# Performance work log

Measured on AMD Instinct MI355X. Metric: run time of the kernel, lower is better.

The kernel has to match this reference:

```python
import jax, jax.numpy as jnp
from jax import lax
import numpy as np

NPOINT1, RADIUS1, NSAMPLE1 = 2048, 0.4, 32
NPOINT2, RADIUS2, NSAMPLE2 = 512, 0.8, 64


def _fps(xyz, npoint):
    # Farthest point sampling (deterministic start at index 0). xyz: (N,3)
    N = xyz.shape[0]
    def step(carry, _):
        dists, farthest = carry
        centroid = xyz[farthest]                      # (3,)
        d = jnp.sum((xyz - centroid) ** 2, axis=-1)   # (N,)
        dists = jnp.minimum(dists, d)
        return (dists, jnp.argmax(dists).astype(jnp.int32)), farthest
    init = (jnp.full((N,), 1e10, xyz.dtype), jnp.asarray(0, jnp.int32))
    _, idx = lax.scan(step, init, None, length=npoint)
    return idx                                        # (npoint,) int32


def _ball_query(radius, nsample, xyz, new_xyz):
    # For each centroid pick up to nsample neighbor indices within radius,
    # padding with the first found index (centroid itself is always in range).
    N = xyz.shape[0]
    sqr = jnp.sum((new_xyz[:, None, :] - xyz[None, :, :]) ** 2, axis=-1)  # (S,N)
    cand = jnp.where(sqr <= radius * radius,
                     jnp.arange(N, dtype=jnp.int32)[None, :], N)
    neg, _ = lax.top_k(-cand, nsample)   # smallest nsample valid indices
    idx = -neg
    first = idx[:, :1]
    return jnp.where(idx == N, first, idx)            # (S, nsample)


def _mlp(h, ws, bs, contract):
    # Per-point shared MLP (1x1 conv + folded-BN bias + ReLU)
    for w, b in zip(ws, bs):
        h = jax.nn.relu(jnp.einsum(contract, h, w) + b)
    return h


def _sa(xyz, feats, npoint, radius, nsample, ws, bs):
    new_xyz = xyz[_fps(xyz, npoint)]                  # (S,3)
    gidx = _ball_query(radius, nsample, xyz, new_xyz) # (S,K)
    grouped_xyz = xyz[gidx] - new_xyz[:, None, :]     # (S,K,3) centered
    h = jnp.concatenate([grouped_xyz, feats[gidx]], axis=-1)  # (S,K,3+C)
    h = _mlp(h, ws, bs, 'skc,oc->sko')
    return new_xyz, jnp.max(h, axis=1)                # (S,C_out)


def _sa_all(xyz, feats, ws, bs):
    # group_all stage: single group over all remaining points
    h = jnp.concatenate([xyz, feats], axis=-1)        # (S,3+C)
    h = _mlp(h, ws, bs, 'sc,oc->so')
    return jnp.max(h, axis=0)                         # (C_out,)


def _forward(points, proposal, w1, b1, w2, b2, w3, b3):
    x, y, w = proposal[0], proposal[1], proposal[3]
    zero = jnp.zeros_like(x)
    xyz = points - jnp.stack([x, y, zero])            # centre-normalized coords
    offs = [(x + w / 2, y), (x - w / 2, y), (x, y + w / 2), (x, y - w / 2)]
    feats = jnp.concatenate(
        [points - jnp.stack([ox, oy, zero]) for ox, oy in offs], axis=-1)  # (N,12)
    xyz1, f1 = _sa(xyz, feats, NPOINT1, RADIUS1, NSAMPLE1, w1, b1)
    xyz2, f2 = _sa(xyz1, f1, NPOINT2, RADIUS2, NSAMPLE2, w2, b2)
    return _sa_all(xyz2, f2, w3, b3)                  # (1024,)


def setup_inputs() -> dict:
    key = jax.random.key(0)
    k = jax.random.split(key, 40)
    N = 32768
    inp = {}
    inp['points'] = jax.random.normal(k[0], (N, 3), jnp.float32)
    inp['proposal'] = jax.random.uniform(k[1], (6,), jnp.float32, 0.1, 1.0)
    dims = {'sa1': [(64, 15), (64, 64), (128, 64)],
            'sa2': [(128, 131), (128, 128), (256, 128)],
            'sa3': [(256, 259), (512, 256), (1024, 512)]}
    ki = 2
    for name, layer_dims in dims.items():
        for i, (o, c) in enumerate(layer_dims):
            inp[f'{name}_w{i}'] = jax.random.normal(k[ki], (o, c), jnp.float32) / np.float32(np.sqrt(c)); ki += 1
            inp[f'{name}_b{i}'] = jax.random.normal(k[ki], (o,), jnp.float32) * 0.02; ki += 1
    return inp


def reference(points, proposal,
              sa1_w0, sa1_w1, sa1_w2, sa1_b0, sa1_b1, sa1_b2,
              sa2_w0, sa2_w1, sa2_w2, sa2_b0, sa2_b1, sa2_b2,
              sa3_w0, sa3_w1, sa3_w2, sa3_b0, sa3_b1, sa3_b2):
    return _forward(points, proposal,
                    [sa1_w0, sa1_w1, sa1_w2], [sa1_b0, sa1_b1, sa1_b2],
                    [sa2_w0, sa2_w1, sa2_w2], [sa2_b0, sa2_b1, sa2_b2],
                    [sa3_w0, sa3_w1, sa3_w2], [sa3_b0, sa3_b1, sa3_b2])
```

## Files before the change

kernel.cpp:

```cpp
#include <hip/hip_runtime.h>
#include <cstdint>
#include <cstddef>

typedef unsigned long long ull;

#define N_PTS  32768
#define NP1    2048
#define NSAMP1 32
#define NP2    512
#define NSAMP2 64

__global__ __launch_bounds__(256) void k_prep(const float* __restrict__ pts,
                                              const float* __restrict__ prop,
                                              float* __restrict__ xx,
                                              float* __restrict__ xy,
                                              float* __restrict__ xz) {
  int t = blockIdx.x * 256 + threadIdx.x;
  if (t >= N_PTS) return;
  float x = prop[0], y = prop[1];
  xx[t] = __fsub_rn(pts[3 * t + 0], x);
  xy[t] = __fsub_rn(pts[3 * t + 1], y);
  xz[t] = pts[3 * t + 2];
}

#define F1T 1024
#define F1P 32

__global__
__attribute__((amdgpu_flat_work_group_size(F1T, F1T)))
void k_fps1(const float* __restrict__ xx,
            const float* __restrict__ xy,
            const float* __restrict__ xz,
            float* __restrict__ ox,
            float* __restrict__ oy,
            float* __restrict__ oz) {
  __shared__ __align__(16) float zl[F1P * F1T];
  __shared__ float wmax[F1T / 64];
  __shared__ int S[2];
  int tid = threadIdx.x;
  char* zb = (char*)zl;
  int rowb = tid * 128 + (tid & 7) * 16;
  float px[F1P], py[F1P], d[F1P];
#pragma unroll
  for (int s = 0; s < F1P; ++s) {
    int i = s * F1T + tid;
    px[s] = xx[i];
    py[s] = xy[i];
    float z = xz[i];
    *(float*)(zb + ((rowb ^ ((s >> 2) * 16)) + (s & 3) * 4)) = z;
    d[s] = 1e10f;
  }
  if (tid == 0) { S[0] = 0; S[1] = 0x7fffffff; }
  __syncthreads();
  for (int it = 0; it < NP1; ++it) {
    int f = __builtin_amdgcn_readfirstlane(S[it & 1]);
    float cx = xx[f], cy = xy[f], cz = xz[f];
    if (tid == 0) { ox[it] = cx; oy[it] = cy; oz[it] = cz; }
    float bestv = -1.0f;
#pragma unroll
    for (int c = 0; c < 8; ++c) {
      const float4 zz = *(const float4*)(zb + (rowb ^ (c * 16)));
      float zv[4] = {zz.x, zz.y, zz.z, zz.w};
#pragma unroll
      for (int j = 0; j < 4; ++j) {
        int s = c * 4 + j;
        float dx = __fsub_rn(px[s], cx);
        float dy = __fsub_rn(py[s], cy);
        float dz = __fsub_rn(zv[j], cz);
        float d2 = __fadd_rn(__fadd_rn(__fmul_rn(dx, dx), __fmul_rn(dy, dy)), __fmul_rn(dz, dz));
        float dn = fminf(d[s], d2);
        d[s] = dn;
        bestv = fmaxf(bestv, dn);
      }
    }
    float wv = bestv;
#pragma unroll
    for (int m = 1; m < 64; m <<= 1) wv = fmaxf(wv, __shfl_xor(wv, m, 64));
    if ((tid & 63) == 0) wmax[tid >> 6] = wv;
    __syncthreads();
    float gb = wmax[0];
#pragma unroll
    for (int k = 1; k < F1T / 64; ++k) gb = fmaxf(gb, wmax[k]);
    if (bestv == gb) {
      int cand = 0x7fffffff;
#pragma unroll
      for (int s = F1P - 1; s >= 0; --s) cand = (d[s] == gb) ? (s * F1T + tid) : cand;
      atomicMin(&S[(it + 1) & 1], cand);
    }
    if (tid == 0) S[it & 1] = 0x7fffffff;
    __syncthreads();
  }
}

#define F2T 512
#define F2P 4
__global__ __launch_bounds__(F2T, 1) void k_fps2(const float* __restrict__ x1x,
                                                 const float* __restrict__ x1y,
                                                 const float* __restrict__ x1z,
                                                 float* __restrict__ ox,
                                                 float* __restrict__ oy,
                                                 float* __restrict__ oz) {
  __shared__ float sx[NP1], sy[NP1], sz[NP1];
  __shared__ float wmax[F2T / 64];
  __shared__ int S[2];
  int tid = threadIdx.x;
  float px[F2P], py[F2P], pz[F2P], d[F2P];
#pragma unroll
  for (int s = 0; s < F2P; ++s) {
    int i = s * F2T + tid;
    px[s] = x1x[i]; py[s] = x1y[i]; pz[s] = x1z[i];
    sx[i] = px[s];  sy[i] = py[s];  sz[i] = pz[s];
    d[s] = 1e10f;
  }
  if (tid == 0) { S[0] = 0; S[1] = 0x7fffffff; }
  __syncthreads();
  for (int it = 0; it < NP2; ++it) {
    int f = __builtin_amdgcn_readfirstlane(S[it & 1]);
    float cx = sx[f], cy = sy[f], cz = sz[f];
    if (tid == 0) { ox[it] = cx; oy[it] = cy; oz[it] = cz; }
    float bestv = -1.0f;
#pragma unroll
    for (int s = 0; s < F2P; ++s) {
      float dx = __fsub_rn(px[s], cx);
      float dy = __fsub_rn(py[s], cy);
      float dz = __fsub_rn(pz[s], cz);
      float d2 = __fadd_rn(__fadd_rn(__fmul_rn(dx, dx), __fmul_rn(dy, dy)), __fmul_rn(dz, dz));
      float dn = fminf(d[s], d2);
      d[s] = dn;
      bestv = fmaxf(bestv, dn);
    }
    float wv = bestv;
#pragma unroll
    for (int m = 1; m < 64; m <<= 1) wv = fmaxf(wv, __shfl_xor(wv, m, 64));
    if ((tid & 63) == 0) wmax[tid >> 6] = wv;
    __syncthreads();
    float gb = wmax[0];
#pragma unroll
    for (int k = 1; k < F2T / 64; ++k) gb = fmaxf(gb, wmax[k]);
    if (bestv == gb) {
      int cand = 0x7fffffff;
#pragma unroll
      for (int s = F2P - 1; s >= 0; --s) cand = (d[s] == gb) ? (s * F2T + tid) : cand;
      atomicMin(&S[(it + 1) & 1], cand);
    }
    if (tid == 0) S[it & 1] = 0x7fffffff;
    __syncthreads();
  }
}

__global__ void k_ballq(const float* __restrict__ px, const float* __restrict__ py,
                        const float* __restrict__ pz, int n,
                        const float* __restrict__ qx, const float* __restrict__ qy,
                        const float* __restrict__ qz, int S,
                        float r2, int ns, int* __restrict__ out) {
  int w = (blockIdx.x * (int)blockDim.x + threadIdx.x) >> 6;
  int lane = threadIdx.x & 63;
  if (w >= S) return;
  float cx = qx[w], cy = qy[w], cz = qz[w];
  int found = 0, first = 0;
  bool havefirst = false;
  for (int base = 0; base < n && found < ns; base += 64) {
    int i = base + lane;
    float dx = __fsub_rn(px[i], cx);
    float dy = __fsub_rn(py[i], cy);
    float dz = __fsub_rn(pz[i], cz);
    float d2 = __fadd_rn(__fadd_rn(__fmul_rn(dx, dx), __fmul_rn(dy, dy)), __fmul_rn(dz, dz));
    bool isin = d2 <= r2;
    ull m = __ballot(isin);
    if (!havefirst && m != 0ull) { first = base + __builtin_ctzll(m); havefirst = true; }
    if (isin) {
      int r = (int)__popcll(m & ((1ull << lane) - 1ull));
      int slot = found + r;
      if (slot < ns) out[w * ns + slot] = i;
    }
    found += (int)__popcll(m);
  }
  for (int s2 = found + lane; s2 < ns; s2 += 64) out[w * ns + s2] = first;
}

__global__ __launch_bounds__(256) void k_gather1(const float* __restrict__ pts,
                                                 const float* __restrict__ prop,
                                                 const float* __restrict__ xx,
                                                 const float* __restrict__ xy,
                                                 const float* __restrict__ xz,
                                                 const float* __restrict__ x1x,
                                                 const float* __restrict__ x1y,
                                                 const float* __restrict__ x1z,
                                                 const int* __restrict__ gidx,
                                                 float* __restrict__ X, int rbase) {
  int rl = blockIdx.x * 256 + threadIdx.x;
  if (rl >= 8192) return;
  int r = rbase + rl;
  int s = r >> 5;
  int g = gidx[r];
  float x = prop[0], y = prop[1], wz = prop[3];
  float w2 = wz * 0.5f;
  float oxp = __fadd_rn(x, w2), oxm = __fsub_rn(x, w2);
  float oyp = __fadd_rn(y, w2), oym = __fsub_rn(y, w2);
  float gx = xx[g], gy = xy[g], gz = xz[g];
  float pxv = pts[3 * g + 0], pyv = pts[3 * g + 1];
  float* o = X + (size_t)rl * 15;
  o[0] = __fsub_rn(gx, x1x[s]);
  o[1] = __fsub_rn(gy, x1y[s]);
  o[2] = __fsub_rn(gz, x1z[s]);
  o[3] = __fsub_rn(pxv, oxp);  o[4]  = gy;                    o[5]  = gz;
  o[6] = __fsub_rn(pxv, oxm);  o[7]  = gy;                    o[8]  = gz;
  o[9] = gx;                   o[10] = __fsub_rn(pyv, oyp);   o[11] = gz;
  o[12] = gx;                  o[13] = __fsub_rn(pyv, oym);   o[14] = gz;
}

__global__ __launch_bounds__(256) void k_gather2(const float* __restrict__ x1x,
                                                 const float* __restrict__ x1y,
                                                 const float* __restrict__ x1z,
                                                 const float* __restrict__ x2x,
                                                 const float* __restrict__ x2y,
                                                 const float* __restrict__ x2z,
                                                 const int* __restrict__ gidx,
                                                 const float* __restrict__ f1,
                                                 float* __restrict__ X, int rbase) {
  int e = blockIdx.x * 256 + threadIdx.x;
  if (e >= 8192 * 131) return;
  int rl = e / 131, c = e % 131;
  int r = rbase + rl;
  int s = r >> 6;
  int g = gidx[r];
  float v;
  if (c == 0)      v = __fsub_rn(x1x[g], x2x[s]);
  else if (c == 1) v = __fsub_rn(x1y[g], x2y[s]);
  else if (c == 2) v = __fsub_rn(x1z[g], x2z[s]);
  else             v = f1[(size_t)g * 128 + (c - 3)];
  X[e] = v;
}

__global__ __launch_bounds__(256) void k_gather3(const float* __restrict__ x2x,
                                                 const float* __restrict__ x2y,
                                                 const float* __restrict__ x2z,
                                                 const float* __restrict__ f2,
                                                 float* __restrict__ X) {
  int e = blockIdx.x * 256 + threadIdx.x;
  if (e >= 512 * 259) return;
  int rl = e / 259, c = e % 259;
  float v;
  if (c == 0)      v = x2x[rl];
  else if (c == 1) v = x2y[rl];
  else if (c == 2) v = x2z[rl];
  else             v = f2[(size_t)rl * 256 + (c - 3)];
  X[e] = v;
}

__global__ __launch_bounds__(256) void k_gemm(const float* __restrict__ A,
                                              const float* __restrict__ W,
                                              const float* __restrict__ bias,
                                              float* __restrict__ C,
                                              int M, int N, int K) {
  __shared__ __align__(16) float As[16][68];
  __shared__ __align__(16) float Bs[16][68];
  int tid = threadIdx.x;
  int bn = blockIdx.x * 64, bm = blockIdx.y * 64;
  int tx = tid & 15, ty = tid >> 4;
  float acc[4][4] = {{0.f, 0.f, 0.f, 0.f}, {0.f, 0.f, 0.f, 0.f},
                     {0.f, 0.f, 0.f, 0.f}, {0.f, 0.f, 0.f, 0.f}};
  for (int k0 = 0; k0 < K; k0 += 16) {
#pragma unroll
    for (int e = 0; e < 4; ++e) {
      int flat = tid + e * 256;
      int rr = flat >> 4, cc = flat & 15;
      As[cc][rr] = (k0 + cc < K) ? A[(size_t)(bm + rr) * K + (k0 + cc)] : 0.0f;
      Bs[cc][rr] = (k0 + cc < K) ? W[(size_t)(bn + rr) * K + (k0 + cc)] : 0.0f;
    }
    __syncthreads();
#pragma unroll
    for (int kk = 0; kk < 16; ++kk) {
      const float4 a = *(const float4*)&As[kk][ty * 4];
      const float4 b = *(const float4*)&Bs[kk][tx * 4];
      float av[4] = {a.x, a.y, a.z, a.w};
      float bb[4] = {b.x, b.y, b.z, b.w};
#pragma unroll
      for (int i = 0; i < 4; ++i)
#pragma unroll
        for (int j = 0; j < 4; ++j)
          acc[i][j] = fmaf(av[i], bb[j], acc[i][j]);
    }
    __syncthreads();
  }
#pragma unroll
  for (int i = 0; i < 4; ++i) {
    int m = bm + ty * 4 + i;
    float4 o;
    o.x = fmaxf(acc[i][0] + bias[bn + tx * 4 + 0], 0.0f);
    o.y = fmaxf(acc[i][1] + bias[bn + tx * 4 + 1], 0.0f);
    o.z = fmaxf(acc[i][2] + bias[bn + tx * 4 + 2], 0.0f);
    o.w = fmaxf(acc[i][3] + bias[bn + tx * 4 + 3], 0.0f);
    *(float4*)&C[(size_t)m * N + bn + tx * 4] = o;
  }
}

__global__ __launch_bounds__(256) void k_maxpool(const float* __restrict__ H,
                                                 float* __restrict__ F,
                                                 int S, int Ks, int Nch, int sbase) {
  int t = blockIdx.x * 256 + threadIdx.x;
  if (t >= S * Nch) return;
  int sl = t / Nch, n = t % Nch;
  const float* p = H + (size_t)sl * Ks * Nch + n;
  float m = p[0];
  for (int k = 1; k < Ks; ++k) m = fmaxf(m, p[(size_t)k * Nch]);
  F[(size_t)(sbase + sl) * Nch + n] = m;
}

extern "C" void kernel_launch(void* const* d_in, const int* in_sizes, int n_in,
                              void* d_out, int out_size, void* d_ws, size_t ws_size,
                              hipStream_t stream) {
  (void)n_in; (void)out_size; (void)ws_size;
  const float* pts = (const float*)d_in[0];
  const float* prop = (const float*)d_in[1];

  bool dict_order = (in_sizes[3] == 64);
  const float *w[3][3], *b[3][3];
  for (int g = 0; g < 3; ++g)
    for (int l = 0; l < 3; ++l) {
      int base = 2 + g * 6;
      int wi = dict_order ? (base + l * 2) : (base + l);
      int bi = dict_order ? (base + l * 2 + 1) : (base + 3 + l);
      w[g][l] = (const float*)d_in[wi];
      b[g][l] = (const float*)d_in[bi];
    }

  float* ws = (float*)d_ws;
  float* xx = ws;
  float* xy = xx + N_PTS;
  float* xz = xy + N_PTS;
  float* x1x = xz + N_PTS;
  float* x1y = x1x + NP1;
  float* x1z = x1y + NP1;
  float* x2x = x1z + NP1;
  float* x2y = x2x + NP2;
  float* x2z = x2y + NP2;
  int* gidx1 = (int*)(x2z + NP2);
  int* gidx2 = gidx1 + NP1 * NSAMP1;
  float* f1 = (float*)(gidx2 + NP2 * NSAMP2);
  float* f2 = f1 + NP1 * 128;
  float* Xp = f2 + NP2 * 256;
  float* Ha = Xp + 8192 * 131;
  float* Hb = Ha + 8192 * 128;
  float* Hc = Hb + 8192 * 128;

  const float R2A = (float)(0.4 * 0.4);
  const float R2B = (float)(0.8 * 0.8);

  k_prep<<<128, 256, 0, stream>>>(pts, prop, xx, xy, xz);
  k_fps1<<<1, F1T, 0, stream>>>(xx, xy, xz, x1x, x1y, x1z);
  k_fps2<<<1, F2T, 0, stream>>>(x1x, x1y, x1z, x2x, x2y, x2z);
  k_ballq<<<512, 256, 0, stream>>>(xx, xy, xz, N_PTS, x1x, x1y, x1z, NP1, R2A, NSAMP1, gidx1);
  k_ballq<<<128, 256, 0, stream>>>(x1x, x1y, x1z, NP1, x2x, x2y, x2z, NP2, R2B, NSAMP2, gidx2);

  for (int ch = 0; ch < 8; ++ch) {
    int rbase = ch * 8192;
    k_gather1<<<32, 256, 0, stream>>>(pts, prop, xx, xy, xz, x1x, x1y, x1z, gidx1, Xp, rbase);
    k_gemm<<<dim3(1, 128), 256, 0, stream>>>(Xp, w[0][0], b[0][0], Ha, 8192, 64, 15);
    k_gemm<<<dim3(1, 128), 256, 0, stream>>>(Ha, w[0][1], b[0][1], Hb, 8192, 64, 64);
    k_gemm<<<dim3(2, 128), 256, 0, stream>>>(Hb, w[0][2], b[0][2], Hc, 8192, 128, 64);
    k_maxpool<<<128, 256, 0, stream>>>(Hc, f1, 256, 32, 128, ch * 256);
  }

  for (int ch = 0; ch < 4; ++ch) {
    int rbase = ch * 8192;
    k_gather2<<<(8192 * 131 + 255) / 256, 256, 0, stream>>>(x1x, x1y, x1z, x2x, x2y, x2z,
                                                            gidx2, f1, Xp, rbase);
    k_gemm<<<dim3(2, 128), 256, 0, stream>>>(Xp, w[1][0], b[1][0], Ha, 8192, 128, 131);
    k_gemm<<<dim3(2, 128), 256, 0, stream>>>(Ha, w[1][1], b[1][1], Hb, 8192, 128, 128);
    k_gemm<<<dim3(4, 128), 256, 0, stream>>>(Hb, w[1][2], b[1][2], Hc, 8192, 256, 128);
    k_maxpool<<<128, 256, 0, stream>>>(Hc, f2, 128, 64, 256, ch * 128);
  }

  k_gather3<<<(512 * 259 + 255) / 256, 256, 0, stream>>>(x2x, x2y, x2z, f2, Xp);
  k_gemm<<<dim3(4, 8), 256, 0, stream>>>(Xp, w[2][0], b[2][0], Ha, 512, 256, 259);
  k_gemm<<<dim3(8, 8), 256, 0, stream>>>(Ha, w[2][1], b[2][1], Hb, 512, 512, 256);
  k_gemm<<<dim3(16, 8), 256, 0, stream>>>(Hb, w[2][2], b[2][2], Hc, 512, 1024, 512);
  k_maxpool<<<4, 256, 0, stream>>>(Hc, (float*)d_out, 1, 512, 1024, 0);
}
```

Before: 5.852 ms.

## Spatially sort points into Morton cells and skip distant FPS updates via bounding boxes

Points are binned into a 16^3 Morton-ordered grid using histogram, scan and scatter kernels, so each FPS thread owns a spatially compact set of 32 points. Each thread keeps a bounding box and skips its distance update when the new centroid's lower-bound distance cannot lower its current max. The block-wide max reduction now uses shuffles, and tie-breaking maps back to original indices through a permutation. This adds several small preprocessing launches and an extra permutation lookup, and tie handling under the reordering could diverge from the reference.

```diff
diff --git a/kernel.cpp b/kernel.cpp
--- a/kernel.cpp
+++ b/kernel.cpp
@@ -9,6 +9,7 @@
 #define NSAMP1 32
 #define NP2    512
 #define NSAMP2 64
+#define NCELL  4096
 
 __global__ __launch_bounds__(256) void k_prep(const float* __restrict__ pts,
                                               const float* __restrict__ prop,
@@ -23,6 +24,75 @@
   xz[t] = pts[3 * t + 2];
 }
 
+__device__ __forceinline__ int spread3(int v) {
+  return (v & 1) | ((v & 2) << 2) | ((v & 4) << 4) | ((v & 8) << 6);
+}
+
+__global__ __launch_bounds__(256) void k_zerocells(int* __restrict__ cellh) {
+  int t = blockIdx.x * 256 + threadIdx.x;
+  if (t < NCELL) cellh[t] = 0;
+}
+
+__global__ __launch_bounds__(256) void k_cell(const float* __restrict__ xx,
+                                              const float* __restrict__ xy,
+                                              const float* __restrict__ xz,
+                                              int* __restrict__ cellid,
+                                              int* __restrict__ cellh) {
+  int t = blockIdx.x * 256 + threadIdx.x;
+  if (t >= N_PTS) return;
+  const float sc = 16.0f / 9.0f;
+  int xi = (int)((xx[t] + 4.5f) * sc); xi = xi < 0 ? 0 : (xi > 15 ? 15 : xi);
+  int yi = (int)((xy[t] + 4.5f) * sc); yi = yi < 0 ? 0 : (yi > 15 ? 15 : yi);
+  int zi = (int)((xz[t] + 4.5f) * sc); zi = zi < 0 ? 0 : (zi > 15 ? 15 : zi);
+  int c = spread3(xi) | (spread3(yi) << 1) | (spread3(zi) << 2);
+  cellid[t] = c;
+  atomicAdd(&cellh[c], 1);
+}
+
+__global__ __launch_bounds__(1024) void k_scan(const int* __restrict__ h,
+                                               int* __restrict__ o) {
+  __shared__ int wsum[16];
+  int tid = threadIdx.x;
+  int4 v = *(const int4*)&h[tid * 4];
+  int s = v.x + v.y + v.z + v.w;
+  int lane = tid & 63;
+  int incl = s;
+#pragma unroll
+  for (int m = 1; m < 64; m <<= 1) {
+    int n = __shfl_up(incl, m, 64);
+    if (lane >= m) incl += n;
+  }
+  if (lane == 63) wsum[tid >> 6] = incl;
+  __syncthreads();
+  int woff = 0;
+  for (int w = 0; w < (tid >> 6); ++w) woff += wsum[w];
+  int excl = woff + incl - s;
+  int4 out;
+  out.x = excl;
+  out.y = excl + v.x;
+  out.z = out.y + v.y;
+  out.w = out.z + v.z;
+  *(int4*)&o[tid * 4] = out;
+}
+
+__global__ __launch_bounds__(256) void k_scatter(const float* __restrict__ xx,
+                                                 const float* __restrict__ xy,
+                                                 const float* __restrict__ xz,
+                                                 const int* __restrict__ cellid,
+                                                 int* __restrict__ cello,
+                                                 float* __restrict__ spx,
+                                                 float* __restrict__ spy,
+                                                 float* __restrict__ spz,
+                                                 int* __restrict__ perm) {
+  int t = blockIdx.x * 256 + threadIdx.x;
+  if (t >= N_PTS) return;
+  int pos = atomicAdd(&cello[cellid[t]], 1);
+  spx[pos] = xx[t];
+  spy[pos] = xy[t];
+  spz[pos] = xz[t];
+  perm[pos] = t;
+}
+
 #define F1T 1024
 #define F1P 32
 
@@ -31,6 +101,10 @@
 void k_fps1(const float* __restrict__ xx,
             const float* __restrict__ xy,
             const float* __restrict__ xz,
+            const float* __restrict__ spx,
+            const float* __restrict__ spy,
+            const float* __restrict__ spz,
+            const int* __restrict__ perm,
             float* __restrict__ ox,
             float* __restrict__ oy,
             float* __restrict__ oz) {
@@ -40,51 +114,65 @@
   int tid = threadIdx.x;
   char* zb = (char*)zl;
   int rowb = tid * 128 + (tid & 7) * 16;
+  int base = tid * F1P;
   float px[F1P], py[F1P], d[F1P];
+  float lox = 1e30f, hix = -1e30f, loy = 1e30f, hiy = -1e30f, loz = 1e30f, hiz = -1e30f;
 #pragma unroll
   for (int s = 0; s < F1P; ++s) {
-    int i = s * F1T + tid;
-    px[s] = xx[i];
-    py[s] = xy[i];
-    float z = xz[i];
+    float x = spx[base + s];
+    float y = spy[base + s];
+    float z = spz[base + s];
+    px[s] = x; py[s] = y;
     *(float*)(zb + ((rowb ^ ((s >> 2) * 16)) + (s & 3) * 4)) = z;
     d[s] = 1e10f;
-  }
+    lox = fminf(lox, x); hix = fmaxf(hix, x);
+    loy = fminf(loy, y); hiy = fmaxf(hiy, y);
+    loz = fminf(loz, z); hiz = fmaxf(hiz, z);
+  }
+  float bmax = 1e10f;
   if (tid == 0) { S[0] = 0; S[1] = 0x7fffffff; }
   __syncthreads();
   for (int it = 0; it < NP1; ++it) {
     int f = __builtin_amdgcn_readfirstlane(S[it & 1]);
     float cx = xx[f], cy = xy[f], cz = xz[f];
     if (tid == 0) { ox[it] = cx; oy[it] = cy; oz[it] = cz; }
-    float bestv = -1.0f;
-#pragma unroll
-    for (int c = 0; c < 8; ++c) {
-      const float4 zz = *(const float4*)(zb + (rowb ^ (c * 16)));
-      float zv[4] = {zz.x, zz.y, zz.z, zz.w};
-#pragma unroll
-      for (int j = 0; j < 4; ++j) {
-        int s = c * 4 + j;
-        float dx = __fsub_rn(px[s], cx);
-        float dy = __fsub_rn(py[s], cy);
-        float dz = __fsub_rn(zv[j], cz);
-        float d2 = __fadd_rn(__fadd_rn(__fmul_rn(dx, dx), __fmul_rn(dy, dy)), __fmul_rn(dz, dz));
-        float dn = fminf(d[s], d2);
-        d[s] = dn;
-        bestv = fmaxf(bestv, dn);
+    float tx = fmaxf(fmaxf(__fsub_rn(lox, cx), __fsub_rn(cx, hix)), 0.0f);
+    float ty = fmaxf(fmaxf(__fsub_rn(loy, cy), __fsub_rn(cy, hiy)), 0.0f);
+    float tz = fmaxf(fmaxf(__fsub_rn(loz, cz), __fsub_rn(cz, hiz)), 0.0f);
+    float lb = __fadd_rn(__fadd_rn(__fmul_rn(tx, tx), __fmul_rn(ty, ty)), __fmul_rn(tz, tz));
+    if (__fmul_rn(lb, 0.9999f) < bmax) {
+      float nb = -1.0f;
+#pragma unroll
+      for (int c = 0; c < 8; ++c) {
+        const float4 zz = *(const float4*)(zb + (rowb ^ (c * 16)));
+        float zv[4] = {zz.x, zz.y, zz.z, zz.w};
+#pragma unroll
+        for (int j = 0; j < 4; ++j) {
+          int s = c * 4 + j;
+          float dx = __fsub_rn(px[s], cx);
+          float dy = __fsub_rn(py[s], cy);
+          float dz = __fsub_rn(zv[j], cz);
+          float d2 = __fadd_rn(__fadd_rn(__fmul_rn(dx, dx), __fmul_rn(dy, dy)), __fmul_rn(dz, dz));
+          float dn = fminf(d[s], d2);
+          d[s] = dn;
+          nb = fmaxf(nb, dn);
+        }
       }
-    }
-    float wv = bestv;
+      bmax = nb;
+    }
+    float wv = bmax;
 #pragma unroll
     for (int m = 1; m < 64; m <<= 1) wv = fmaxf(wv, __shfl_xor(wv, m, 64));
     if ((tid & 63) == 0) wmax[tid >> 6] = wv;
     __syncthreads();
-    float gb = wmax[0];
-#pragma unroll
-    for (int k = 1; k < F1T / 64; ++k) gb = fmaxf(gb, wmax[k]);
-    if (bestv == gb) {
+    float gb = wmax[tid & 15];
+#pragma unroll
+    for (int m = 1; m < 16; m <<= 1) gb = fmaxf(gb, __shfl_xor(gb, m, 64));
+    if (bmax == gb) {
       int cand = 0x7fffffff;
 #pragma unroll
-      for (int s = F1P - 1; s >= 0; --s) cand = (d[s] == gb) ? (s * F1T + tid) : cand;
+      for (int s = 0; s < F1P; ++s)
+        if (d[s] == gb) { int oi = perm[base + s]; cand = cand < oi ? cand : oi; }
       atomicMin(&S[(it + 1) & 1], cand);
     }
     if (tid == 0) S[it & 1] = 0x7fffffff;
@@ -344,11 +432,23 @@
   float* Hb = Ha + 8192 * 128;
   float* Hc = Hb + 8192 * 128;
 
+  int*   cellid = (int*)Xp;
+  int*   cellh  = cellid + N_PTS;
+  int*   cello  = cellh + NCELL;
+  int*   perm   = cello + NCELL;
+  float* spx    = (float*)(perm + N_PTS);
+  float* spy    = spx + N_PTS;
+  float* spz    = spy + N_PTS;
+
   const float R2A = (float)(0.4 * 0.4);
   const float R2B = (float)(0.8 * 0.8);
 
   k_prep<<<128, 256, 0, stream>>>(pts, prop, xx, xy, xz);
-  k_fps1<<<1, F1T, 0, stream>>>(xx, xy, xz, x1x, x1y, x1z);
+  k_zerocells<<<16, 256, 0, stream>>>(cellh);
+  k_cell<<<128, 256, 0, stream>>>(xx, xy, xz, cellid, cellh);
+  k_scan<<<1, 1024, 0, stream>>>(cellh, cello);
+  k_scatter<<<128, 256, 0, stream>>>(xx, xy, xz, cellid, cello, spx, spy, spz, perm);
+  k_fps1<<<1, F1T, 0, stream>>>(xx, xy, xz, spx, spy, spz, perm, x1x, x1y, x1z);
   k_fps2<<<1, F2T, 0, stream>>>(x1x, x1y, x1z, x2x, x2y, x2z);
   k_ballq<<<512, 256, 0, stream>>>(xx, xy, xz, N_PTS, x1x, x1y, x1z, NP1, R2A, NSAMP1, gidx1);
   k_ballq<<<128, 256, 0, stream>>>(x1x, x1y, x1z, NP1, x2x, x2y, x2z, NP2, R2B, NSAMP2, gidx2);
```

After: 9.551 ms. 1.63x slower.
